# Kernel tuning notes

Measured on AMD Instinct MI355X. Metric: run time of the kernel, lower is better.

Reference implementation:

```python
import jax, jax.numpy as jnp
import numpy as np

DIM = 2048
N_HEADS = 32
N_KV_HEADS = 8
HEAD_DIM = DIM // N_HEADS  # 64
N_REP = N_HEADS // N_KV_HEADS  # 4
B, S = 1, 2048


def _rope(t, cos, sin):
    # t: (b, s, h, head_dim); cos/sin: (s, head_dim//2)
    tr = t.reshape(*t.shape[:-1], -1, 2)
    a, b = tr[..., 0], tr[..., 1]
    c = cos[None, :, None, :]
    s_ = sin[None, :, None, :]
    ra = a * c - b * s_
    rb = a * s_ + b * c
    return jnp.stack([ra, rb], axis=-1).reshape(t.shape)


def setup_inputs() -> dict:
    key = jax.random.key(0)
    ks = jax.random.split(key, 6)
    sc = 1.0 / np.sqrt(DIM)
    x = jax.random.normal(ks[0], (B, S, DIM), dtype=jnp.float32)
    wq = jax.random.normal(ks[1], (DIM, N_HEADS * HEAD_DIM), dtype=jnp.float32) * sc
    wk = jax.random.normal(ks[2], (DIM, N_KV_HEADS * HEAD_DIM), dtype=jnp.float32) * sc
    wv = jax.random.normal(ks[3], (DIM, N_KV_HEADS * HEAD_DIM), dtype=jnp.float32) * sc
    wo = jax.random.normal(ks[4], (N_HEADS * HEAD_DIM, DIM), dtype=jnp.float32) * sc
    # rotary frequencies (theta = 500000 as in Llama3)
    inv = 1.0 / (500000.0 ** (np.arange(0, HEAD_DIM, 2, dtype=np.float32) / HEAD_DIM))
    ang = np.arange(S, dtype=np.float32)[:, None] * inv[None, :]
    freqs_cos = jnp.asarray(np.cos(ang), dtype=jnp.float32)
    freqs_sin = jnp.asarray(np.sin(ang), dtype=jnp.float32)
    # causal additive mask
    mask = jnp.triu(jnp.full((S, S), -1e9, dtype=jnp.float32), k=1)
    return {"x": x, "wq": wq, "wk": wk, "wv": wv, "wo": wo,
            "freqs_cos": freqs_cos, "freqs_sin": freqs_sin, "mask": mask,
            "start_pos": 0}


def reference(x, wq, wk, wv, wo, freqs_cos, freqs_sin, mask, start_pos):
    b, s, _ = x.shape
    xq = (x @ wq).reshape(b, s, N_HEADS, HEAD_DIM)
    xk = (x @ wk).reshape(b, s, N_KV_HEADS, HEAD_DIM)
    xv = (x @ wv).reshape(b, s, N_KV_HEADS, HEAD_DIM)
    xq = _rope(xq, freqs_cos, freqs_sin)
    xk = _rope(xk, freqs_cos, freqs_sin)
    # GQA without repeat_interleave: view queries as (b, s, kv, rep, d)
    q = xq.reshape(b, s, N_KV_HEADS, N_REP, HEAD_DIM)
    scale = 1.0 / np.sqrt(HEAD_DIM)
    # scores: (b, kv, rep, q, k)
    scores = jnp.einsum('bqkrd,bskd->bkrqs', q, xk) * scale
    scores = scores + mask[None, None, None, :, :]
    probs = jax.nn.softmax(scores.astype(jnp.float32), axis=-1).astype(x.dtype)
    out = jnp.einsum('bkrqs,bskd->bqkrd', probs, xv)
    out = out.reshape(b, s, N_HEADS * HEAD_DIM)
    return out @ wo
```

## Files before the change

### kernel.cpp

```cpp
#include <hip/hip_runtime.h>
#include <hip/hip_bf16.h>

#define DIM 2048
#define S_LEN 2048
#define N_HEADS 32
#define N_KV_HEADS 8
#define HEAD_DIM 64
#define KV_DIM (N_KV_HEADS * HEAD_DIM)
#define QKV_N (DIM + 2 * KV_DIM)
#define QSCALE 0.18033688011112042f

typedef __attribute__((ext_vector_type(8))) short bf16x8;
typedef __attribute__((ext_vector_type(4))) float f32x4;

__device__ __forceinline__ unsigned short bf16_of(float f) {
    __hip_bfloat16 h = __float2bfloat16(f);
    return *reinterpret_cast<unsigned short*>(&h);
}
__device__ __forceinline__ float f_of_bf16(unsigned short u) {
    unsigned int x = ((unsigned int)u) << 16;
    return __uint_as_float(x);
}
__device__ __forceinline__ void gl_lds16(const void* g, void* l) {
    __builtin_amdgcn_global_load_lds((const __attribute__((address_space(1))) void*)g,
                                     (__attribute__((address_space(3))) void*)l, 16, 0, 0);
}
__device__ __forceinline__ unsigned int pack2bf(float a, float b) {
    return (unsigned int)bf16_of(a) | ((unsigned int)bf16_of(b) << 16);
}

__global__ __launch_bounds__(256) void convert_x(const float* __restrict__ src,
                                                 unsigned short* __restrict__ dst) {
    int idx = blockIdx.x * 256 + threadIdx.x;
    float4 f = ((const float4*)src)[idx];
    ushort4 u;
    u.x = bf16_of(f.x); u.y = bf16_of(f.y); u.z = bf16_of(f.z); u.w = bf16_of(f.w);
    ((ushort4*)dst)[idx] = u;
}

__global__ __launch_bounds__(256) void transpose_cvt(const float* __restrict__ src,
                                                     unsigned short* __restrict__ dst,
                                                     int src_cols, int dst_stride) {
    __shared__ float tile[64][65];
    const int c0 = blockIdx.x * 64;
    const int r0 = blockIdx.y * 64;
    const int t = threadIdx.x;
#pragma unroll
    for (int i = 0; i < 16; i++) {
        int idx = t + i * 256;
        int r = idx >> 6, c = idx & 63;
        tile[r][c] = src[(size_t)(r0 + r) * src_cols + c0 + c];
    }
    __syncthreads();
#pragma unroll
    for (int i = 0; i < 16; i++) {
        int idx = t + i * 256;
        int r = idx >> 6, c = idx & 63;
        dst[(size_t)(c0 + r) * dst_stride + r0 + c] = bf16_of(tile[c][r]);
    }
}

__global__ __launch_bounds__(256) void gemm_bt(const unsigned short* __restrict__ A,
                                               const unsigned short* __restrict__ Bt,
                                               void* __restrict__ Cv,
                                               int M, int N, int K, int c_bf16) {
    __shared__ unsigned short As[128 * 64];
    __shared__ unsigned short Bs[128 * 64];
    const int tid = threadIdx.x;
    const int wave = tid >> 6, lane = tid & 63;
    const int m16 = lane & 15, quad = lane >> 4;
    const int m0 = blockIdx.y * 128, n0 = blockIdx.x * 128;
    const int wm = (wave >> 1) * 64, wn = (wave & 1) * 64;

    const int lrow = lane >> 3;
    const int gc = (lane & 7) ^ lrow;
    const unsigned short* Ab = A + (size_t)(m0 + wave * 8 + lrow) * K + gc * 8;
    const unsigned short* Bb = Bt + (size_t)(n0 + wave * 8 + lrow) * K + gc * 8;

    f32x4 acc[4][4];
#pragma unroll
    for (int mb = 0; mb < 4; mb++)
#pragma unroll
        for (int nb = 0; nb < 4; nb++) acc[mb][nb] = (f32x4){0.f, 0.f, 0.f, 0.f};

    for (int k0 = 0; k0 < K; k0 += 64) {
#pragma unroll
        for (int g = 0; g < 4; g++) {
            gl_lds16(Ab + (size_t)g * 32 * K + k0, &As[(g * 32 + wave * 8) * 64]);
            gl_lds16(Bb + (size_t)g * 32 * K + k0, &Bs[(g * 32 + wave * 8) * 64]);
        }
        __syncthreads();
#pragma unroll
        for (int ks = 0; ks < 2; ks++) {
            bf16x8 af[4], bfr[4];
#pragma unroll
            for (int mb = 0; mb < 4; mb++) {
                int row = wm + mb * 16 + m16;
                int ch = (ks * 4 + quad) ^ (m16 & 7);
                af[mb] = *(const bf16x8*)&As[row * 64 + ch * 8];
                int rowb = wn + mb * 16 + m16;
                bfr[mb] = *(const bf16x8*)&Bs[rowb * 64 + ch * 8];
            }
#pragma unroll
            for (int mb = 0; mb < 4; mb++)
#pragma unroll
                for (int nb = 0; nb < 4; nb++)
                    acc[mb][nb] = __builtin_amdgcn_mfma_f32_16x16x32_bf16(af[mb], bfr[nb], acc[mb][nb], 0, 0, 0);
        }
        __syncthreads();
    }

    if (c_bf16) {
        unsigned short* C = (unsigned short*)Cv;
#pragma unroll
        for (int mb = 0; mb < 4; mb++)
#pragma unroll
            for (int nb = 0; nb < 4; nb++)
#pragma unroll
                for (int r = 0; r < 4; r++)
                    C[(size_t)(m0 + wm + mb * 16 + quad * 4 + r) * N + n0 + wn + nb * 16 + m16] =
                        bf16_of(acc[mb][nb][r]);
    } else {
        float* C = (float*)Cv;
#pragma unroll
        for (int mb = 0; mb < 4; mb++)
#pragma unroll
            for (int nb = 0; nb < 4; nb++)
#pragma unroll
                for (int r = 0; r < 4; r++)
                    C[(size_t)(m0 + wm + mb * 16 + quad * 4 + r) * N + n0 + wn + nb * 16 + m16] =
                        acc[mb][nb][r];
    }
}

__global__ __launch_bounds__(256) void rope_bf16(const unsigned short* __restrict__ qkv,
                                                 unsigned short* __restrict__ qbf,
                                                 unsigned short* __restrict__ kbf,
                                                 const float* __restrict__ fcos,
                                                 const float* __restrict__ fsin) {
    int idx = blockIdx.x * 256 + threadIdx.x;
    const int nq = S_LEN * N_HEADS * 8;
    int s, j, srcoff, dstoff;
    unsigned short* dst;
    float osc;
    if (idx < nq) {
        s = idx >> 8;
        int rem = idx & 255;
        int h = rem >> 3;
        j = rem & 7;
        srcoff = s * QKV_N + h * 64 + j * 8;
        dstoff = s * DIM + h * 64 + j * 8;
        dst = qbf;
        osc = QSCALE;
    } else {
        int t2 = idx - nq;
        s = t2 >> 6;
        int rem = t2 & 63;
        int h = rem >> 3;
        j = rem & 7;
        srcoff = s * QKV_N + DIM + h * 64 + j * 8;
        dstoff = s * KV_DIM + h * 64 + j * 8;
        dst = kbf;
        osc = 1.0f;
    }
    bf16x8 v8 = *(const bf16x8*)&qkv[srcoff];
    float4 c4 = *(const float4*)&fcos[s * 32 + j * 4];
    float4 s4 = *(const float4*)&fsin[s * 32 + j * 4];
    float cs[4] = {c4.x, c4.y, c4.z, c4.w};
    float sn[4] = {s4.x, s4.y, s4.z, s4.w};
    bf16x8 o;
#pragma unroll
    for (int p = 0; p < 4; p++) {
        float a = f_of_bf16((unsigned short)v8[2 * p]);
        float b = f_of_bf16((unsigned short)v8[2 * p + 1]);
        o[2 * p]     = (short)bf16_of((a * cs[p] - b * sn[p]) * osc);
        o[2 * p + 1] = (short)bf16_of((a * sn[p] + b * cs[p]) * osc);
    }
    *(bf16x8*)&dst[dstoff] = o;
}

__global__ __launch_bounds__(256) void transpose_v_bf16(const unsigned short* __restrict__ qkv,
                                                        unsigned short* __restrict__ vbt) {
    __shared__ unsigned short tile[64][65];
    const int d0 = blockIdx.x * 64;
    const int s0 = blockIdx.y * 64;
    const int t = threadIdx.x;
#pragma unroll
    for (int i = 0; i < 16; i++) {
        int idx = t + i * 256;
        int r = idx >> 6, c = idx & 63;
        tile[r][c] = qkv[(size_t)(s0 + r) * QKV_N + DIM + KV_DIM + d0 + c];
    }
    __syncthreads();
#pragma unroll
    for (int i = 0; i < 16; i++) {
        int idx = t + i * 256;
        int r = idx >> 6, c = idx & 63;
        int key = s0 + c;
        int kl = key & 127;
        int kp = (kl & 0x60) | ((kl & 0x0C) << 1) | ((kl & 0x10) >> 2) | (kl & 3);
        vbt[(size_t)(d0 + r) * S_LEN + (key & ~127) + kp] = tile[c][r];
    }
}

__global__ __launch_bounds__(256) void attn_mfma3(const unsigned short* __restrict__ qb,
                                                  const unsigned short* __restrict__ kb,
                                                  const unsigned short* __restrict__ vbt,
                                                  unsigned short* __restrict__ out) {
    const int h  = blockIdx.y;
    const int bx = blockIdx.x;
    const int kh = h >> 2;
    const int tid  = threadIdx.x;
    const int wave = tid >> 6;
    const int lane = tid & 63;
    const int m16  = lane & 15;
    const int quad = lane >> 4;

    __shared__ unsigned short Ks[128 * 64];
    __shared__ unsigned short Vt[64 * 128];

    const int lrow8 = lane >> 3;
    const int kc    = (lane & 7) ^ lrow8;
    const int lrow4 = lane >> 4;
    const int vc    = (lane & 15) ^ ((wave * 4 + lrow4) & 7);

    const unsigned short* Kbase = kb + (size_t)kh * 64 + (size_t)(wave * 8 + lrow8) * KV_DIM + kc * 8;
    const unsigned short* Vbase = vbt + (size_t)(kh * 64 + wave * 4 + lrow4) * S_LEN + vc * 8;

#pragma unroll
    for (int half = 0; half < 2; half++) {
        const int qt = half ? bx : (31 - bx);
        const int q0 = qt * 64;
        const int n_iter = (qt >> 1) + 1;

        bf16x8 qa[2];
        {
            const int qrow = q0 + wave * 16 + m16;
#pragma unroll
            for (int ks = 0; ks < 2; ks++)
                qa[ks] = *(const bf16x8*)&qb[(size_t)qrow * DIM + h * 64 + ks * 32 + quad * 8];
        }

        f32x4 o_acc[4];
#pragma unroll
        for (int nb = 0; nb < 4; nb++) o_acc[nb] = (f32x4){0.f, 0.f, 0.f, 0.f};
        float m_s = -1e30f, l_s = 0.f;
        const int qrow_lane = q0 + wave * 16 + m16;
        const int orow_base = q0 + wave * 16 + quad * 4;

        for (int kt = 0; kt < n_iter; kt++) {
#pragma unroll
            for (int g = 0; g < 4; g++) {
                gl_lds16(Kbase + (size_t)(kt * 128 + g * 32) * KV_DIM, &Ks[(g * 32 + wave * 8) * 64]);
                gl_lds16(Vbase + (size_t)g * 16 * S_LEN + kt * 128, &Vt[(g * 16 + wave * 4) * 128]);
            }
            __syncthreads();

            f32x4 sc[8];
#pragma unroll
            for (int cb = 0; cb < 8; cb++) sc[cb] = (f32x4){0.f, 0.f, 0.f, 0.f};
#pragma unroll
            for (int ks = 0; ks < 2; ks++) {
                const int slot = (ks * 4 + quad) ^ (m16 & 7);
#pragma unroll
                for (int cb = 0; cb < 8; cb++) {
                    bf16x8 kf = *(const bf16x8*)&Ks[(cb * 16 + m16) * 64 + slot * 8];
                    sc[cb] = __builtin_amdgcn_mfma_f32_16x16x32_bf16(kf, qa[ks], sc[cb], 0, 0, 0);
                }
            }

            if (kt == n_iter - 1) {
#pragma unroll
                for (int cb = 0; cb < 8; cb++) {
                    int key = kt * 128 + cb * 16 + quad * 4;
#pragma unroll
                    for (int r = 0; r < 4; r++)
                        if (key + r > qrow_lane) sc[cb][r] = -1e30f;
                }
            }

            float rmax = sc[0][0];
#pragma unroll
            for (int cb = 0; cb < 8; cb++)
#pragma unroll
                for (int r = 0; r < 4; r++) rmax = fmaxf(rmax, sc[cb][r]);
            rmax = fmaxf(rmax, __shfl_xor(rmax, 16, 64));
            rmax = fmaxf(rmax, __shfl_xor(rmax, 32, 64));

            float mnew = fmaxf(m_s, rmax);
            float alpha = __builtin_amdgcn_exp2f(m_s - mnew);
            m_s = mnew;

            float rsum = 0.f;
#pragma unroll
            for (int cb = 0; cb < 8; cb++)
#pragma unroll
                for (int r = 0; r < 4; r++) {
                    float p = __builtin_amdgcn_exp2f(sc[cb][r] - mnew);
                    sc[cb][r] = p;
                    rsum += p;
                }
            rsum += __shfl_xor(rsum, 16, 64);
            rsum += __shfl_xor(rsum, 32, 64);
            l_s = l_s * alpha + rsum;

            unsigned int P01[8], P23[8];
#pragma unroll
            for (int cb = 0; cb < 8; cb++) {
                P01[cb] = pack2bf(sc[cb][0], sc[cb][1]);
                P23[cb] = pack2bf(sc[cb][2], sc[cb][3]);
            }

#pragma unroll
            for (int r = 0; r < 4; r++) {
                float a_r = __shfl(alpha, quad * 4 + r, 64);
#pragma unroll
                for (int nb = 0; nb < 4; nb++) o_acc[nb][r] *= a_r;
            }

#pragma unroll
            for (int ks = 0; ks < 4; ks++) {
                union { unsigned int u[4]; bf16x8 v; } pa;
                pa.u[0] = P01[2 * ks];     pa.u[1] = P23[2 * ks];
                pa.u[2] = P01[2 * ks + 1]; pa.u[3] = P23[2 * ks + 1];
                const int slot = (ks * 4 + quad) ^ (m16 & 7);
#pragma unroll
                for (int nb = 0; nb < 4; nb++) {
                    bf16x8 vf = *(const bf16x8*)&Vt[(nb * 16 + m16) * 128 + slot * 8];
                    o_acc[nb] = __builtin_amdgcn_mfma_f32_16x16x32_bf16(pa.v, vf, o_acc[nb], 0, 0, 0);
                }
            }
            __syncthreads();
        }

#pragma unroll
        for (int r = 0; r < 4; r++) {
            float l_r = __shfl(l_s, quad * 4 + r, 64);
            float inv_l = 1.f / l_r;
#pragma unroll
            for (int nb = 0; nb < 4; nb++)
                out[(size_t)(orow_base + r) * DIM + h * 64 + nb * 16 + m16] =
                    bf16_of(o_acc[nb][r] * inv_l);
        }
    }
}

extern "C" void kernel_launch(void* const* d_in, const int* in_sizes, int n_in,
                              void* d_out, int out_size, void* d_ws, size_t ws_size,
                              hipStream_t stream) {
    const float* x    = (const float*)d_in[0];
    const float* wq   = (const float*)d_in[1];
    const float* wk   = (const float*)d_in[2];
    const float* wv   = (const float*)d_in[3];
    const float* wo   = (const float*)d_in[4];
    const float* fcos = (const float*)d_in[5];
    const float* fsin = (const float*)d_in[6];

    char* ws = (char*)d_ws;
    const size_t MB = 1024 * 1024;
    unsigned short* xbf    = (unsigned short*)(ws);
    unsigned short* wqkvT  = (unsigned short*)(ws + 8 * MB);
    unsigned short* woT    = (unsigned short*)(ws + 20 * MB);
    unsigned short* qkvbf  = (unsigned short*)(ws + 28 * MB);
    unsigned short* vbt    = (unsigned short*)(ws + 40 * MB);
    unsigned short* qbf    = (unsigned short*)(ws + 8 * MB);
    unsigned short* kbf    = (unsigned short*)(ws + 16 * MB);
    unsigned short* attnbf = (unsigned short*)(ws);

    convert_x<<<(DIM * S_LEN / 4) / 256, 256, 0, stream>>>(x, xbf);
    transpose_cvt<<<dim3(32, 32), 256, 0, stream>>>(wq, wqkvT, DIM, DIM);
    transpose_cvt<<<dim3(8, 32), 256, 0, stream>>>(wk, wqkvT + (size_t)DIM * DIM, KV_DIM, DIM);
    transpose_cvt<<<dim3(8, 32), 256, 0, stream>>>(wv, wqkvT + (size_t)(DIM + KV_DIM) * DIM, KV_DIM, DIM);
    transpose_cvt<<<dim3(32, 32), 256, 0, stream>>>(wo, woT, DIM, DIM);

    gemm_bt<<<dim3(QKV_N / 128, S_LEN / 128), 256, 0, stream>>>(xbf, wqkvT, qkvbf,
                                                                S_LEN, QKV_N, DIM, 1);

    int n_chunks = S_LEN * N_HEADS * 8 + S_LEN * N_KV_HEADS * 8;
    rope_bf16<<<n_chunks / 256, 256, 0, stream>>>(qkvbf, qbf, kbf, fcos, fsin);

    transpose_v_bf16<<<dim3(KV_DIM / 64, S_LEN / 64), 256, 0, stream>>>(qkvbf, vbt);

    attn_mfma3<<<dim3(16, N_HEADS), 256, 0, stream>>>(qbf, kbf, vbt, attnbf);

    gemm_bt<<<dim3(DIM / 128, S_LEN / 128), 256, 0, stream>>>(attnbf, woT, d_out,
                                                              S_LEN, DIM, DIM, 0);
}
```

Before: 259.1 us.

## Split attention KV range across two blocks, merge launches, narrow GEMM tiles

Fuses the five weight/input conversion launches into one prep kernel and merges RoPE with the V transpose, which cuts launch overhead. GEMM tiles shrink from 128x128 to 128x64 so more blocks fill the GPU. Attention now splits each query tile's key range into two parts (split-K flash style), each writing partial outputs plus max/sum stats, and a new combine kernel merges them. This raises attention parallelism at the cost of extra partial-output traffic and an additional kernel.

```diff
diff --git a/kernel.cpp b/kernel.cpp
--- a/kernel.cpp
+++ b/kernel.cpp
@@ -29,22 +29,34 @@
     return (unsigned int)bf16_of(a) | ((unsigned int)bf16_of(b) << 16);
 }
 
-__global__ __launch_bounds__(256) void convert_x(const float* __restrict__ src,
-                                                 unsigned short* __restrict__ dst) {
-    int idx = blockIdx.x * 256 + threadIdx.x;
-    float4 f = ((const float4*)src)[idx];
-    ushort4 u;
-    u.x = bf16_of(f.x); u.y = bf16_of(f.y); u.z = bf16_of(f.z); u.w = bf16_of(f.w);
-    ((ushort4*)dst)[idx] = u;
-}
-
-__global__ __launch_bounds__(256) void transpose_cvt(const float* __restrict__ src,
-                                                     unsigned short* __restrict__ dst,
-                                                     int src_cols, int dst_stride) {
+__global__ __launch_bounds__(256) void prep(const float* __restrict__ x,
+                                            const float* __restrict__ wq,
+                                            const float* __restrict__ wk,
+                                            const float* __restrict__ wv,
+                                            const float* __restrict__ wo,
+                                            unsigned short* __restrict__ xbf,
+                                            unsigned short* __restrict__ wqkvT,
+                                            unsigned short* __restrict__ woT) {
     __shared__ float tile[64][65];
-    const int c0 = blockIdx.x * 64;
-    const int r0 = blockIdx.y * 64;
     const int t = threadIdx.x;
+    int b = blockIdx.x;
+    if (b < 4096) {
+        int idx = b * 256 + t;
+        float4 f = ((const float4*)x)[idx];
+        ushort4 u;
+        u.x = bf16_of(f.x); u.y = bf16_of(f.y); u.z = bf16_of(f.z); u.w = bf16_of(f.w);
+        ((ushort4*)xbf)[idx] = u;
+        return;
+    }
+    b -= 4096;
+    const float* src;
+    unsigned short* dst;
+    int src_cols, bx, by;
+    if (b < 1024)      { src = wq; dst = wqkvT;                                src_cols = DIM;    bx = b & 31;          by = b >> 5; }
+    else if (b < 1280) { src = wk; dst = wqkvT + (size_t)DIM * DIM;            src_cols = KV_DIM; bx = (b - 1024) & 7;  by = (b - 1024) >> 3; }
+    else if (b < 1536) { src = wv; dst = wqkvT + (size_t)(DIM + KV_DIM) * DIM; src_cols = KV_DIM; bx = (b - 1280) & 7;  by = (b - 1280) >> 3; }
+    else               { src = wo; dst = woT;                                  src_cols = DIM;    bx = (b - 1536) & 31; by = (b - 1536) >> 5; }
+    const int c0 = bx * 64, r0 = by * 64;
 #pragma unroll
     for (int i = 0; i < 16; i++) {
         int idx = t + i * 256;
@@ -56,55 +68,55 @@
     for (int i = 0; i < 16; i++) {
         int idx = t + i * 256;
         int r = idx >> 6, c = idx & 63;
-        dst[(size_t)(c0 + r) * dst_stride + r0 + c] = bf16_of(tile[c][r]);
-    }
-}
-
-__global__ __launch_bounds__(256) void gemm_bt(const unsigned short* __restrict__ A,
-                                               const unsigned short* __restrict__ Bt,
-                                               void* __restrict__ Cv,
-                                               int M, int N, int K, int c_bf16) {
+        dst[(size_t)(c0 + r) * DIM + r0 + c] = bf16_of(tile[c][r]);
+    }
+}
+
+__global__ __launch_bounds__(256) void gemm_bt64(const unsigned short* __restrict__ A,
+                                                 const unsigned short* __restrict__ Bt,
+                                                 void* __restrict__ Cv,
+                                                 int M, int N, int K, int c_bf16) {
     __shared__ unsigned short As[128 * 64];
-    __shared__ unsigned short Bs[128 * 64];
+    __shared__ unsigned short Bs[64 * 64];
     const int tid = threadIdx.x;
     const int wave = tid >> 6, lane = tid & 63;
     const int m16 = lane & 15, quad = lane >> 4;
-    const int m0 = blockIdx.y * 128, n0 = blockIdx.x * 128;
-    const int wm = (wave >> 1) * 64, wn = (wave & 1) * 64;
+    const int m0 = blockIdx.y * 128, n0 = blockIdx.x * 64;
+    const int wm = (wave >> 1) * 64, wn = (wave & 1) * 32;
 
     const int lrow = lane >> 3;
     const int gc = (lane & 7) ^ lrow;
     const unsigned short* Ab = A + (size_t)(m0 + wave * 8 + lrow) * K + gc * 8;
     const unsigned short* Bb = Bt + (size_t)(n0 + wave * 8 + lrow) * K + gc * 8;
 
-    f32x4 acc[4][4];
+    f32x4 acc[4][2];
 #pragma unroll
     for (int mb = 0; mb < 4; mb++)
 #pragma unroll
-        for (int nb = 0; nb < 4; nb++) acc[mb][nb] = (f32x4){0.f, 0.f, 0.f, 0.f};
+        for (int nb = 0; nb < 2; nb++) acc[mb][nb] = (f32x4){0.f, 0.f, 0.f, 0.f};
 
     for (int k0 = 0; k0 < K; k0 += 64) {
 #pragma unroll
-        for (int g = 0; g < 4; g++) {
+        for (int g = 0; g < 4; g++)
             gl_lds16(Ab + (size_t)g * 32 * K + k0, &As[(g * 32 + wave * 8) * 64]);
+#pragma unroll
+        for (int g = 0; g < 2; g++)
             gl_lds16(Bb + (size_t)g * 32 * K + k0, &Bs[(g * 32 + wave * 8) * 64]);
-        }
         __syncthreads();
 #pragma unroll
         for (int ks = 0; ks < 2; ks++) {
-            bf16x8 af[4], bfr[4];
-#pragma unroll
-            for (int mb = 0; mb < 4; mb++) {
-                int row = wm + mb * 16 + m16;
-                int ch = (ks * 4 + quad) ^ (m16 & 7);
-                af[mb] = *(const bf16x8*)&As[row * 64 + ch * 8];
-                int rowb = wn + mb * 16 + m16;
-                bfr[mb] = *(const bf16x8*)&Bs[rowb * 64 + ch * 8];
-            }
+            const int ch = (ks * 4 + quad) ^ (m16 & 7);
+            bf16x8 af[4], bfr[2];
 #pragma unroll
             for (int mb = 0; mb < 4; mb++)
-#pragma unroll
-                for (int nb = 0; nb < 4; nb++)
+                af[mb] = *(const bf16x8*)&As[(wm + mb * 16 + m16) * 64 + ch * 8];
+#pragma unroll
+            for (int nb = 0; nb < 2; nb++)
+                bfr[nb] = *(const bf16x8*)&Bs[(wn + nb * 16 + m16) * 64 + ch * 8];
+#pragma unroll
+            for (int mb = 0; mb < 4; mb++)
+#pragma unroll
+                for (int nb = 0; nb < 2; nb++)
                     acc[mb][nb] = __builtin_amdgcn_mfma_f32_16x16x32_bf16(af[mb], bfr[nb], acc[mb][nb], 0, 0, 0);
         }
         __syncthreads();
@@ -115,7 +127,7 @@
 #pragma unroll
         for (int mb = 0; mb < 4; mb++)
 #pragma unroll
-            for (int nb = 0; nb < 4; nb++)
+            for (int nb = 0; nb < 2; nb++)
 #pragma unroll
                 for (int r = 0; r < 4; r++)
                     C[(size_t)(m0 + wm + mb * 16 + quad * 4 + r) * N + n0 + wn + nb * 16 + m16] =
@@ -125,7 +137,7 @@
 #pragma unroll
         for (int mb = 0; mb < 4; mb++)
 #pragma unroll
-            for (int nb = 0; nb < 4; nb++)
+            for (int nb = 0; nb < 2; nb++)
 #pragma unroll
                 for (int r = 0; r < 4; r++)
                     C[(size_t)(m0 + wm + mb * 16 + quad * 4 + r) * N + n0 + wn + nb * 16 + m16] =
@@ -133,58 +145,60 @@
     }
 }
 
-__global__ __launch_bounds__(256) void rope_bf16(const unsigned short* __restrict__ qkv,
-                                                 unsigned short* __restrict__ qbf,
-                                                 unsigned short* __restrict__ kbf,
-                                                 const float* __restrict__ fcos,
-                                                 const float* __restrict__ fsin) {
-    int idx = blockIdx.x * 256 + threadIdx.x;
-    const int nq = S_LEN * N_HEADS * 8;
-    int s, j, srcoff, dstoff;
-    unsigned short* dst;
-    float osc;
-    if (idx < nq) {
-        s = idx >> 8;
-        int rem = idx & 255;
-        int h = rem >> 3;
-        j = rem & 7;
-        srcoff = s * QKV_N + h * 64 + j * 8;
-        dstoff = s * DIM + h * 64 + j * 8;
-        dst = qbf;
-        osc = QSCALE;
-    } else {
-        int t2 = idx - nq;
-        s = t2 >> 6;
-        int rem = t2 & 63;
-        int h = rem >> 3;
-        j = rem & 7;
-        srcoff = s * QKV_N + DIM + h * 64 + j * 8;
-        dstoff = s * KV_DIM + h * 64 + j * 8;
-        dst = kbf;
-        osc = 1.0f;
-    }
-    bf16x8 v8 = *(const bf16x8*)&qkv[srcoff];
-    float4 c4 = *(const float4*)&fcos[s * 32 + j * 4];
-    float4 s4 = *(const float4*)&fsin[s * 32 + j * 4];
-    float cs[4] = {c4.x, c4.y, c4.z, c4.w};
-    float sn[4] = {s4.x, s4.y, s4.z, s4.w};
-    bf16x8 o;
-#pragma unroll
-    for (int p = 0; p < 4; p++) {
-        float a = f_of_bf16((unsigned short)v8[2 * p]);
-        float b = f_of_bf16((unsigned short)v8[2 * p + 1]);
-        o[2 * p]     = (short)bf16_of((a * cs[p] - b * sn[p]) * osc);
-        o[2 * p + 1] = (short)bf16_of((a * sn[p] + b * cs[p]) * osc);
-    }
-    *(bf16x8*)&dst[dstoff] = o;
-}
-
-__global__ __launch_bounds__(256) void transpose_v_bf16(const unsigned short* __restrict__ qkv,
-                                                        unsigned short* __restrict__ vbt) {
+__global__ __launch_bounds__(256) void rope_tv(const unsigned short* __restrict__ qkv,
+                                               unsigned short* __restrict__ qbf,
+                                               unsigned short* __restrict__ kbf,
+                                               unsigned short* __restrict__ vbt,
+                                               const float* __restrict__ fcos,
+                                               const float* __restrict__ fsin) {
     __shared__ unsigned short tile[64][65];
-    const int d0 = blockIdx.x * 64;
-    const int s0 = blockIdx.y * 64;
     const int t = threadIdx.x;
+    int b = blockIdx.x;
+    if (b < 2560) {
+        int idx = b * 256 + t;
+        const int nq = S_LEN * N_HEADS * 8;
+        int s, j, srcoff, dstoff;
+        unsigned short* dst;
+        float osc;
+        if (idx < nq) {
+            s = idx >> 8;
+            int rem = idx & 255;
+            int h = rem >> 3;
+            j = rem & 7;
+            srcoff = s * QKV_N + h * 64 + j * 8;
+            dstoff = s * DIM + h * 64 + j * 8;
+            dst = qbf;
+            osc = QSCALE;
+        } else {
+            int t2 = idx - nq;
+            s = t2 >> 6;
+            int rem = t2 & 63;
+            int h = rem >> 3;
+            j = rem & 7;
+            srcoff = s * QKV_N + DIM + h * 64 + j * 8;
+            dstoff = s * KV_DIM + h * 64 + j * 8;
+            dst = kbf;
+            osc = 1.0f;
+        }
+        bf16x8 v8 = *(const bf16x8*)&qkv[srcoff];
+        float4 c4 = *(const float4*)&fcos[s * 32 + j * 4];
+        float4 s4 = *(const float4*)&fsin[s * 32 + j * 4];
+        float cs[4] = {c4.x, c4.y, c4.z, c4.w};
+        float sn[4] = {s4.x, s4.y, s4.z, s4.w};
+        bf16x8 o;
+#pragma unroll
+        for (int p = 0; p < 4; p++) {
+            float a = f_of_bf16((unsigned short)v8[2 * p]);
+            float bb = f_of_bf16((unsigned short)v8[2 * p + 1]);
+            o[2 * p]     = (short)bf16_of((a * cs[p] - bb * sn[p]) * osc);
+            o[2 * p + 1] = (short)bf16_of((a * sn[p] + bb * cs[p]) * osc);
+        }
+        *(bf16x8*)&dst[dstoff] = o;
+        return;
+    }
+    b -= 2560;
+    const int d0 = (b & 7) * 64;
+    const int s0 = (b >> 3) * 64;
 #pragma unroll
     for (int i = 0; i < 16; i++) {
         int idx = t + i * 256;
@@ -203,12 +217,16 @@
     }
 }
 
-__global__ __launch_bounds__(256) void attn_mfma3(const unsigned short* __restrict__ qb,
+__global__ __launch_bounds__(256) void attn_mfma4(const unsigned short* __restrict__ qb,
                                                   const unsigned short* __restrict__ kb,
                                                   const unsigned short* __restrict__ vbt,
-                                                  unsigned short* __restrict__ out) {
-    const int h  = blockIdx.y;
-    const int bx = blockIdx.x;
+                                                  unsigned short* __restrict__ O0,
+                                                  unsigned short* __restrict__ O1,
+                                                  float2* __restrict__ ml0,
+                                                  float2* __restrict__ ml1) {
+    const int bx   = blockIdx.x;
+    const int part = blockIdx.y;
+    const int h    = blockIdx.z;
     const int kh = h >> 2;
     const int tid  = threadIdx.x;
     const int wave = tid >> 6;
@@ -216,6 +234,9 @@
     const int m16  = lane & 15;
     const int quad = lane >> 4;
 
+    unsigned short* Op = part ? O1 : O0;
+    float2* mlp = part ? ml1 : ml0;
+
     __shared__ unsigned short Ks[128 * 64];
     __shared__ unsigned short Vt[64 * 128];
 
@@ -231,7 +252,10 @@
     for (int half = 0; half < 2; half++) {
         const int qt = half ? bx : (31 - bx);
         const int q0 = qt * 64;
-        const int n_iter = (qt >> 1) + 1;
+        const int n_full = (qt >> 1) + 1;
+        const int n0 = (n_full + 1) >> 1;
+        const int kt_lo = part ? n0 : 0;
+        const int kt_hi = part ? n_full : n0;
 
         bf16x8 qa[2];
         {
@@ -248,7 +272,7 @@
         const int qrow_lane = q0 + wave * 16 + m16;
         const int orow_base = q0 + wave * 16 + quad * 4;
 
-        for (int kt = 0; kt < n_iter; kt++) {
+        for (int kt = kt_lo; kt < kt_hi; kt++) {
 #pragma unroll
             for (int g = 0; g < 4; g++) {
                 gl_lds16(Kbase + (size_t)(kt * 128 + g * 32) * KV_DIM, &Ks[(g * 32 + wave * 8) * 64]);
@@ -269,7 +293,7 @@
                 }
             }
 
-            if (kt == n_iter - 1) {
+            if (kt == n_full - 1) {
 #pragma unroll
                 for (int cb = 0; cb < 8; cb++) {
                     int key = kt * 128 + cb * 16 + quad * 4;
@@ -336,13 +360,40 @@
 #pragma unroll
         for (int r = 0; r < 4; r++) {
             float l_r = __shfl(l_s, quad * 4 + r, 64);
-            float inv_l = 1.f / l_r;
+            float inv_l = (l_r > 0.f) ? (1.f / l_r) : 0.f;
 #pragma unroll
             for (int nb = 0; nb < 4; nb++)
-                out[(size_t)(orow_base + r) * DIM + h * 64 + nb * 16 + m16] =
+                Op[(size_t)(orow_base + r) * DIM + h * 64 + nb * 16 + m16] =
                     bf16_of(o_acc[nb][r] * inv_l);
         }
-    }
+        if (quad == 0)
+            mlp[h * S_LEN + q0 + wave * 16 + m16] = make_float2(m_s, l_s);
+    }
+}
+
+__global__ __launch_bounds__(256) void combine(unsigned short* __restrict__ O0,
+                                               const unsigned short* __restrict__ O1,
+                                               const float2* __restrict__ ml0,
+                                               const float2* __restrict__ ml1) {
+    int idx = blockIdx.x * 256 + threadIdx.x;
+    int row = idx >> 9;
+    int cc = (idx & 511) * 4;
+    int h = cc >> 6;
+    float2 a0 = ml0[h * S_LEN + row];
+    float2 a1 = ml1[h * S_LEN + row];
+    float m = fmaxf(a0.x, a1.x);
+    float w0 = a0.y * __builtin_amdgcn_exp2f(a0.x - m);
+    float w1 = a1.y * __builtin_amdgcn_exp2f(a1.x - m);
+    float inv = 1.f / (w0 + w1);
+    w0 *= inv; w1 *= inv;
+    ushort4 u0 = *(const ushort4*)&O0[(size_t)row * DIM + cc];
+    ushort4 u1 = *(const ushort4*)&O1[(size_t)row * DIM + cc];
+    ushort4 o;
+    o.x = bf16_of(w0 * f_of_bf16(u0.x) + w1 * f_of_bf16(u1.x));
+    o.y = bf16_of(w0 * f_of_bf16(u0.y) + w1 * f_of_bf16(u1.y));
+    o.z = bf16_of(w0 * f_of_bf16(u0.z) + w1 * f_of_bf16(u1.z));
+    o.w = bf16_of(w0 * f_of_bf16(u0.w) + w1 * f_of_bf16(u1.w));
+    *(ushort4*)&O0[(size_t)row * DIM + cc] = o;
 }
 
 extern "C" void kernel_launch(void* const* d_in, const int* in_sizes, int n_in,
@@ -363,26 +414,25 @@
     unsigned short* woT    = (unsigned short*)(ws + 20 * MB);
     unsigned short* qkvbf  = (unsigned short*)(ws + 28 * MB);
     unsigned short* vbt    = (unsigned short*)(ws + 40 * MB);
+    float2*         ml0    = (float2*)(ws + 42 * MB);
+    float2*         ml1    = (float2*)(ws + 42 * MB + 512 * 1024);
     unsigned short* qbf    = (unsigned short*)(ws + 8 * MB);
     unsigned short* kbf    = (unsigned short*)(ws + 16 * MB);
-    unsigned short* attnbf = (unsigned short*)(ws);
-
-    convert_x<<<(DIM * S_LEN / 4) / 256, 256, 0, stream>>>(x, xbf);
-    transpose_cvt<<<dim3(32, 32), 256, 0, stream>>>(wq, wqkvT, DIM, DIM);
-    transpose_cvt<<<dim3(8, 32), 256, 0, stream>>>(wk, wqkvT + (size_t)DIM * DIM, KV_DIM, DIM);
-    transpose_cvt<<<dim3(8, 32), 256, 0, stream>>>(wv, wqkvT + (size_t)(DIM + KV_DIM) * DIM, KV_DIM, DIM);
-    transpose_cvt<<<dim3(32, 32), 256, 0, stream>>>(wo, woT, DIM, DIM);
-
-    gemm_bt<<<dim3(QKV_N / 128, S_LEN / 128), 256, 0, stream>>>(xbf, wqkvT, qkvbf,
-                                                                S_LEN, QKV_N, DIM, 1);
-
-    int n_chunks = S_LEN * N_HEADS * 8 + S_LEN * N_KV_HEADS * 8;
-    rope_bf16<<<n_chunks / 256, 256, 0, stream>>>(qkvbf, qbf, kbf, fcos, fsin);
-
-    transpose_v_bf16<<<dim3(KV_DIM / 64, S_LEN / 64), 256, 0, stream>>>(qkvbf, vbt);
-
-    attn_mfma3<<<dim3(16, N_HEADS), 256, 0, stream>>>(qbf, kbf, vbt, attnbf);
-
-    gemm_bt<<<dim3(DIM / 128, S_LEN / 128), 256, 0, stream>>>(attnbf, woT, d_out,
-                                                              S_LEN, DIM, DIM, 0);
-}
+    unsigned short* Opart0 = (unsigned short*)(ws);
+    unsigned short* Opart1 = (unsigned short*)(ws + 28 * MB);
+
+    prep<<<4096 + 2560, 256, 0, stream>>>(x, wq, wk, wv, wo, xbf, wqkvT, woT);
+
+    gemm_bt64<<<dim3(QKV_N / 64, S_LEN / 128), 256, 0, stream>>>(xbf, wqkvT, qkvbf,
+                                                                 S_LEN, QKV_N, DIM, 1);
+
+    rope_tv<<<2560 + 256, 256, 0, stream>>>(qkvbf, qbf, kbf, vbt, fcos, fsin);
+
+    attn_mfma4<<<dim3(16, 2, N_HEADS), 256, 0, stream>>>(qbf, kbf, vbt,
+                                                         Opart0, Opart1, ml0, ml1);
+
+    combine<<<(S_LEN * DIM / 4) / 256, 256, 0, stream>>>(Opart0, Opart1, ml0, ml1);
+
+    gemm_bt64<<<dim3(DIM / 64, S_LEN / 128), 256, 0, stream>>>(Opart0, woT, d_out,
+                                                               S_LEN, DIM, DIM, 0);
+}
```

Measured after the change: 238.7 us. 1.09x faster.
